# Kernel tuning notes

Measured on AMD Instinct MI355X. Metric: run time of the kernel, lower is better.

## Reference

```python
import jax, jax.numpy as jnp
import numpy as np

WIDTH = 1024

def setup_inputs() -> dict:
    key = jax.random.key(0)
    ks = jax.random.split(key, 5)
    x = jax.random.normal(ks[0], (4, 4096, WIDTH), dtype=jnp.float32)
    # LayerNorm params
    ln_gamma = jnp.ones((WIDTH,), dtype=jnp.float32)
    ln_beta = jnp.zeros((WIDTH,), dtype=jnp.float32)
    # Linear params (torch nn.Linear init: U(-1/sqrt(fan_in), 1/sqrt(fan_in)))
    bound = 1.0 / np.sqrt(WIDTH)
    w1 = jax.random.uniform(ks[1], (WIDTH, WIDTH), jnp.float32, -bound, bound)
    b1 = jax.random.uniform(ks[2], (WIDTH,), jnp.float32, -bound, bound)
    w2 = jax.random.uniform(ks[3], (WIDTH, WIDTH), jnp.float32, -bound, bound)
    b2 = jax.random.uniform(ks[4], (WIDTH,), jnp.float32, -bound, bound)
    return {"x": x, "ln_gamma": ln_gamma, "ln_beta": ln_beta,
            "w1": w1, "b1": b1, "w2": w2, "b2": b2}

def _layernorm(x, gamma, beta, eps=1e-5):
    mu = jnp.mean(x, axis=-1, keepdims=True)
    var = jnp.mean(jnp.square(x - mu), axis=-1, keepdims=True)
    return (x - mu) * jax.lax.rsqrt(var + eps) * gamma + beta

def reference(x, ln_gamma, ln_beta, w1, b1, w2, b2):
    # Pre-norm residual MLP: x + W2 @ gelu(W1 @ LN(x) + b1) + b2
    h = _layernorm(x, ln_gamma, ln_beta)
    h = jnp.einsum('bsd,ed->bse', h, w1) + b1  # w stored as [out, in] like torch
    h = jax.nn.gelu(h, approximate=False)      # torch nn.GELU default = exact erf
    # dropout p=0.0 -> identity
    h = jnp.einsum('bsd,ed->bse', h, w2) + b2
    return x + h
```

## Files before the change

kernel.cpp:

```cpp
#include <hip/hip_runtime.h>
#include <hip/hip_bf16.h>
#include <math.h>

typedef __bf16 bf16x8 __attribute__((ext_vector_type(8)));
typedef float f32x4 __attribute__((ext_vector_type(4)));

#define GAS __attribute__((address_space(1)))
#define LAS __attribute__((address_space(3)))

static __device__ __forceinline__ void load16(const void* g, void* l) {
    __builtin_amdgcn_global_load_lds((const GAS void*)g, (LAS void*)l, 16, 0, 0);
}

struct __align__(8) bh4 { __hip_bfloat16 x, y, z, w; };

__global__ __launch_bounds__(256) void ln_kernel(
        const float* __restrict__ x, const float* __restrict__ gamma,
        const float* __restrict__ beta, __hip_bfloat16* __restrict__ out) {
    const int row  = (blockIdx.x << 2) + (threadIdx.x >> 6);
    const int lane = threadIdx.x & 63;
    const float4* px = (const float4*)(x + (size_t)row * 1024);
    float4 v[4];
    float s = 0.f;
#pragma unroll
    for (int i = 0; i < 4; ++i) {
        v[i] = px[lane + (i << 6)];
        s += v[i].x + v[i].y + v[i].z + v[i].w;
    }
#pragma unroll
    for (int o = 32; o; o >>= 1) s += __shfl_xor(s, o, 64);
    const float mu = s * (1.0f / 1024.0f);
    float vs = 0.f;
#pragma unroll
    for (int i = 0; i < 4; ++i) {
        float a = v[i].x - mu, b = v[i].y - mu, c = v[i].z - mu, d = v[i].w - mu;
        vs += a * a + b * b + c * c + d * d;
    }
#pragma unroll
    for (int o = 32; o; o >>= 1) vs += __shfl_xor(vs, o, 64);
    const float rs = rsqrtf(vs * (1.0f / 1024.0f) + 1e-5f);
    const float4* pg = (const float4*)gamma;
    const float4* pb = (const float4*)beta;
    bh4* po = (bh4*)(out + (size_t)row * 1024);
#pragma unroll
    for (int i = 0; i < 4; ++i) {
        const int idx = lane + (i << 6);
        float4 g = pg[idx], bb = pb[idx];
        bh4 r;
        r.x = __float2bfloat16((v[i].x - mu) * rs * g.x + bb.x);
        r.y = __float2bfloat16((v[i].y - mu) * rs * g.y + bb.y);
        r.z = __float2bfloat16((v[i].z - mu) * rs * g.z + bb.z);
        r.w = __float2bfloat16((v[i].w - mu) * rs * g.w + bb.w);
        po[idx] = r;
    }
}

__global__ __launch_bounds__(256) void cvt_kernel(
        const float* __restrict__ w1, const float* __restrict__ w2,
        __hip_bfloat16* __restrict__ o1, __hip_bfloat16* __restrict__ o2) {
    const int i = blockIdx.x * 256 + threadIdx.x;
    float4 a = ((const float4*)w1)[i];
    float4 b = ((const float4*)w2)[i];
    bh4 r1, r2;
    r1.x = __float2bfloat16(a.x); r1.y = __float2bfloat16(a.y);
    r1.z = __float2bfloat16(a.z); r1.w = __float2bfloat16(a.w);
    r2.x = __float2bfloat16(b.x); r2.y = __float2bfloat16(b.y);
    r2.z = __float2bfloat16(b.z); r2.w = __float2bfloat16(b.w);
    ((bh4*)o1)[i] = r1;
    ((bh4*)o2)[i] = r2;
}

template <int EPI>
__global__ __launch_bounds__(256) void gemm_kernel(
        const __hip_bfloat16* __restrict__ A,
        const __hip_bfloat16* __restrict__ B,
        const float* __restrict__ bias,
        const float* __restrict__ resid,
        __hip_bfloat16* __restrict__ outb,
        float* __restrict__ outf) {
    constexpr int K = 1024, N = 1024;
    __shared__ __align__(16) __hip_bfloat16 sA[128 * 32];
    __shared__ __align__(16) __hip_bfloat16 sB[128 * 32];

    const int tid  = threadIdx.x;
    const int lane = tid & 63;
    const int w    = tid >> 6;
    const int wm   = (w >> 1) * 64;
    const int wn   = (w & 1) * 64;
    const int bm   = blockIdx.y * 128;
    const int bn   = blockIdx.x * 128;

    const int lr = tid >> 2;
    const int lc = (tid & 3) * 8;
    const __hip_bfloat16* ga = A + (size_t)(bm + lr) * K + lc;
    const __hip_bfloat16* gb = B + (size_t)(bn + lr) * K + lc;
    char* la = (char*)sA + tid * 16;
    char* lb = (char*)sB + tid * 16;

    f32x4 acc[4][4] = {};

    const int fr = lane & 15;
    const int fk = (lane >> 4) * 8;

    for (int kt = 0; kt < K; kt += 32) {
        load16(ga + kt,                 la);
        load16(ga + kt + (size_t)64*K,  la + 4096);
        load16(gb + kt,                 lb);
        load16(gb + kt + (size_t)64*K,  lb + 4096);
        __syncthreads();
        bf16x8 af[4], bfr[4];
#pragma unroll
        for (int i = 0; i < 4; ++i) {
            af[i]  = *(const bf16x8*)&sA[(wm + i * 16 + fr) * 32 + fk];
            bfr[i] = *(const bf16x8*)&sB[(wn + i * 16 + fr) * 32 + fk];
        }
#pragma unroll
        for (int i = 0; i < 4; ++i)
#pragma unroll
            for (int j = 0; j < 4; ++j)
                acc[i][j] = __builtin_amdgcn_mfma_f32_16x16x32_bf16(af[i], bfr[j], acc[i][j], 0, 0, 0);
        __syncthreads();
    }

    const int cr = (lane >> 4) * 4;
    const int cc = lane & 15;
#pragma unroll
    for (int i = 0; i < 4; ++i) {
#pragma unroll
        for (int r = 0; r < 4; ++r) {
            const size_t grow = (size_t)(bm + wm + i * 16 + cr + r);
#pragma unroll
            for (int j = 0; j < 4; ++j) {
                const int gcol = bn + wn + j * 16 + cc;
                float v = acc[i][j][r] + bias[gcol];
                if (EPI == 0) {
                    float g = 0.5f * v * (1.0f + erff(v * 0.70710678118654752f));
                    outb[grow * N + gcol] = __float2bfloat16(g);
                } else {
                    outf[grow * N + gcol] = v + resid[grow * N + gcol];
                }
            }
        }
    }
}

extern "C" void kernel_launch(void* const* d_in, const int* in_sizes, int n_in,
                              void* d_out, int out_size, void* d_ws, size_t ws_size,
                              hipStream_t stream) {
    const float* x     = (const float*)d_in[0];
    const float* gamma = (const float*)d_in[1];
    const float* beta  = (const float*)d_in[2];
    const float* w1    = (const float*)d_in[3];
    const float* b1    = (const float*)d_in[4];
    const float* w2    = (const float*)d_in[5];
    const float* b2    = (const float*)d_in[6];
    float* out = (float*)d_out;

    const int M = in_sizes[0] / 1024;

    char* ws = (char*)d_ws;
    __hip_bfloat16* hn  = (__hip_bfloat16*)ws;
    __hip_bfloat16* h1  = (__hip_bfloat16*)(ws + (size_t)M * 2048);
    __hip_bfloat16* w1b = (__hip_bfloat16*)(ws + (size_t)M * 4096);
    __hip_bfloat16* w2b = (__hip_bfloat16*)(ws + (size_t)M * 4096 + 2097152);

    ln_kernel<<<M / 4, 256, 0, stream>>>(x, gamma, beta, hn);
    cvt_kernel<<<1024, 256, 0, stream>>>(w1, w2, w1b, w2b);
    gemm_kernel<0><<<dim3(8, M / 128), 256, 0, stream>>>(hn, w1b, b1, nullptr, h1, nullptr);
    gemm_kernel<1><<<dim3(8, M / 128), 256, 0, stream>>>(h1, w2b, b2, x, nullptr, out);
}
```

Measured before the change: 255.1 us.

## Fuse prep kernels, deepen GEMM K-tile, swizzle LDS layout, vectorize epilogue

Merges the LayerNorm and weight-conversion kernels into one launch. The GEMM now uses a 64-wide K tile with an LDS layout that matches the MFMA fragments, so fragment loads become contiguous per-lane 16-byte reads. B rows are permuted so each lane owns four consecutive output columns, which allows vectorized bias, residual and output accesses. The grid axes are swapped so consecutive blocks walk along M, and launch bounds request 4 blocks per CU. Doubling LDS to 32KB per block may limit occupancy.

```diff
diff --git a/kernel.cpp b/kernel.cpp
--- a/kernel.cpp
+++ b/kernel.cpp
@@ -14,9 +14,24 @@
 
 struct __align__(8) bh4 { __hip_bfloat16 x, y, z, w; };
 
-__global__ __launch_bounds__(256) void ln_kernel(
+__global__ __launch_bounds__(256) void pre_kernel(
         const float* __restrict__ x, const float* __restrict__ gamma,
-        const float* __restrict__ beta, __hip_bfloat16* __restrict__ out) {
+        const float* __restrict__ beta, const float* __restrict__ w1,
+        const float* __restrict__ w2, __hip_bfloat16* __restrict__ hn,
+        __hip_bfloat16* __restrict__ w1b, __hip_bfloat16* __restrict__ w2b, int nln) {
+    if ((int)blockIdx.x >= nln) {
+        const int i = (blockIdx.x - nln) * 256 + threadIdx.x;
+        float4 a = ((const float4*)w1)[i];
+        float4 b = ((const float4*)w2)[i];
+        bh4 r1, r2;
+        r1.x = __float2bfloat16(a.x); r1.y = __float2bfloat16(a.y);
+        r1.z = __float2bfloat16(a.z); r1.w = __float2bfloat16(a.w);
+        r2.x = __float2bfloat16(b.x); r2.y = __float2bfloat16(b.y);
+        r2.z = __float2bfloat16(b.z); r2.w = __float2bfloat16(b.w);
+        ((bh4*)w1b)[i] = r1;
+        ((bh4*)w2b)[i] = r2;
+        return;
+    }
     const int row  = (blockIdx.x << 2) + (threadIdx.x >> 6);
     const int lane = threadIdx.x & 63;
     const float4* px = (const float4*)(x + (size_t)row * 1024);
@@ -41,7 +56,7 @@
     const float rs = rsqrtf(vs * (1.0f / 1024.0f) + 1e-5f);
     const float4* pg = (const float4*)gamma;
     const float4* pb = (const float4*)beta;
-    bh4* po = (bh4*)(out + (size_t)row * 1024);
+    bh4* po = (bh4*)(hn + (size_t)row * 1024);
 #pragma unroll
     for (int i = 0; i < 4; ++i) {
         const int idx = lane + (i << 6);
@@ -55,23 +70,8 @@
     }
 }
 
-__global__ __launch_bounds__(256) void cvt_kernel(
-        const float* __restrict__ w1, const float* __restrict__ w2,
-        __hip_bfloat16* __restrict__ o1, __hip_bfloat16* __restrict__ o2) {
-    const int i = blockIdx.x * 256 + threadIdx.x;
-    float4 a = ((const float4*)w1)[i];
-    float4 b = ((const float4*)w2)[i];
-    bh4 r1, r2;
-    r1.x = __float2bfloat16(a.x); r1.y = __float2bfloat16(a.y);
-    r1.z = __float2bfloat16(a.z); r1.w = __float2bfloat16(a.w);
-    r2.x = __float2bfloat16(b.x); r2.y = __float2bfloat16(b.y);
-    r2.z = __float2bfloat16(b.z); r2.w = __float2bfloat16(b.w);
-    ((bh4*)o1)[i] = r1;
-    ((bh4*)o2)[i] = r2;
-}
-
 template <int EPI>
-__global__ __launch_bounds__(256) void gemm_kernel(
+__global__ __launch_bounds__(256, 4) void gemm_kernel(
         const __hip_bfloat16* __restrict__ A,
         const __hip_bfloat16* __restrict__ B,
         const float* __restrict__ bias,
@@ -79,66 +79,82 @@
         __hip_bfloat16* __restrict__ outb,
         float* __restrict__ outf) {
     constexpr int K = 1024, N = 1024;
-    __shared__ __align__(16) __hip_bfloat16 sA[128 * 32];
-    __shared__ __align__(16) __hip_bfloat16 sB[128 * 32];
+    __shared__ __align__(16) char sA[16384];
+    __shared__ __align__(16) char sB[16384];
 
     const int tid  = threadIdx.x;
     const int lane = tid & 63;
     const int w    = tid >> 6;
     const int wm   = (w >> 1) * 64;
     const int wn   = (w & 1) * 64;
-    const int bm   = blockIdx.y * 128;
-    const int bn   = blockIdx.x * 128;
+    const int bm   = blockIdx.x * 128;
+    const int bn   = blockIdx.y * 128;
 
-    const int lr = tid >> 2;
-    const int lc = (tid & 3) * 8;
-    const __hip_bfloat16* ga = A + (size_t)(bm + lr) * K + lc;
-    const __hip_bfloat16* gb = B + (size_t)(bn + lr) * K + lc;
-    char* la = (char*)sA + tid * 16;
-    char* lb = (char*)sB + tid * 16;
+    const int f = lane & 15;
+    const int h = lane >> 4;
+
+    const __hip_bfloat16* gA[4];
+    const __hip_bfloat16* gB[4];
+#pragma unroll
+    for (int q = 0; q < 4; ++q) {
+        const int u  = q * 4 + w;
+        const int rg = u >> 1, c = u & 1;
+        gA[q] = A + (size_t)(bm + rg * 16 + f) * K + c * 32 + h * 8;
+        const int cg = u >> 3, j = (u >> 1) & 3;
+        gB[q] = B + (size_t)(bn + cg * 64 + f * 4 + j) * K + c * 32 + h * 8;
+    }
+    char* lA = sA + tid * 16;
+    char* lB = sB + tid * 16;
 
     f32x4 acc[4][4] = {};
 
-    const int fr = lane & 15;
-    const int fk = (lane >> 4) * 8;
-
-    for (int kt = 0; kt < K; kt += 32) {
-        load16(ga + kt,                 la);
-        load16(ga + kt + (size_t)64*K,  la + 4096);
-        load16(gb + kt,                 lb);
-        load16(gb + kt + (size_t)64*K,  lb + 4096);
+    for (int kt = 0; kt < K; kt += 64) {
+#pragma unroll
+        for (int q = 0; q < 4; ++q) {
+            load16(gA[q] + kt, lA + q * 4096);
+            load16(gB[q] + kt, lB + q * 4096);
+        }
         __syncthreads();
-        bf16x8 af[4], bfr[4];
 #pragma unroll
-        for (int i = 0; i < 4; ++i) {
-            af[i]  = *(const bf16x8*)&sA[(wm + i * 16 + fr) * 32 + fk];
-            bfr[i] = *(const bf16x8*)&sB[(wn + i * 16 + fr) * 32 + fk];
-        }
+        for (int c = 0; c < 2; ++c) {
+            bf16x8 af[4], bf[4];
 #pragma unroll
-        for (int i = 0; i < 4; ++i)
+            for (int i = 0; i < 4; ++i)
+                af[i] = *(const bf16x8*)(sA + ((((wm >> 4) + i) * 2 + c) << 10) + lane * 16);
 #pragma unroll
             for (int j = 0; j < 4; ++j)
-                acc[i][j] = __builtin_amdgcn_mfma_f32_16x16x32_bf16(af[i], bfr[j], acc[i][j], 0, 0, 0);
+                bf[j] = *(const bf16x8*)(sB + ((((wn >> 4) + j) * 2 + c) << 10) + lane * 16);
+#pragma unroll
+            for (int i = 0; i < 4; ++i)
+#pragma unroll
+                for (int j = 0; j < 4; ++j)
+                    acc[i][j] = __builtin_amdgcn_mfma_f32_16x16x32_bf16(af[i], bf[j], acc[i][j], 0, 0, 0);
+        }
         __syncthreads();
     }
 
-    const int cr = (lane >> 4) * 4;
-    const int cc = lane & 15;
+    const float4 bias4 = *(const float4*)(bias + bn + wn + f * 4);
+    const int colb = bn + wn + f * 4;
 #pragma unroll
     for (int i = 0; i < 4; ++i) {
 #pragma unroll
         for (int r = 0; r < 4; ++r) {
-            const size_t grow = (size_t)(bm + wm + i * 16 + cr + r);
-#pragma unroll
-            for (int j = 0; j < 4; ++j) {
-                const int gcol = bn + wn + j * 16 + cc;
-                float v = acc[i][j][r] + bias[gcol];
-                if (EPI == 0) {
-                    float g = 0.5f * v * (1.0f + erff(v * 0.70710678118654752f));
-                    outb[grow * N + gcol] = __float2bfloat16(g);
-                } else {
-                    outf[grow * N + gcol] = v + resid[grow * N + gcol];
-                }
+            const size_t grow = (size_t)(bm + wm + i * 16 + h * 4 + r);
+            float v0 = acc[i][0][r] + bias4.x;
+            float v1 = acc[i][1][r] + bias4.y;
+            float v2 = acc[i][2][r] + bias4.z;
+            float v3 = acc[i][3][r] + bias4.w;
+            if (EPI == 0) {
+                bh4 o;
+                o.x = __float2bfloat16(0.5f * v0 * (1.0f + erff(v0 * 0.70710678118654752f)));
+                o.y = __float2bfloat16(0.5f * v1 * (1.0f + erff(v1 * 0.70710678118654752f)));
+                o.z = __float2bfloat16(0.5f * v2 * (1.0f + erff(v2 * 0.70710678118654752f)));
+                o.w = __float2bfloat16(0.5f * v3 * (1.0f + erff(v3 * 0.70710678118654752f)));
+                *(bh4*)(outb + grow * N + colb) = o;
+            } else {
+                const float4 rs = *(const float4*)(resid + grow * N + colb);
+                float4 o = {v0 + rs.x, v1 + rs.y, v2 + rs.z, v3 + rs.w};
+                *(float4*)(outf + grow * N + colb) = o;
             }
         }
     }
@@ -164,8 +180,8 @@
     __hip_bfloat16* w1b = (__hip_bfloat16*)(ws + (size_t)M * 4096);
     __hip_bfloat16* w2b = (__hip_bfloat16*)(ws + (size_t)M * 4096 + 2097152);
 
-    ln_kernel<<<M / 4, 256, 0, stream>>>(x, gamma, beta, hn);
-    cvt_kernel<<<1024, 256, 0, stream>>>(w1, w2, w1b, w2b);
-    gemm_kernel<0><<<dim3(8, M / 128), 256, 0, stream>>>(hn, w1b, b1, nullptr, h1, nullptr);
-    gemm_kernel<1><<<dim3(8, M / 128), 256, 0, stream>>>(h1, w2b, b2, x, nullptr, out);
+    const int nln = M / 4;
+    pre_kernel<<<nln + 1024, 256, 0, stream>>>(x, gamma, beta, w1, w2, hn, w1b, w2b, nln);
+    gemm_kernel<0><<<dim3(M / 128, 8), 256, 0, stream>>>(hn, w1b, b1, nullptr, h1, nullptr);
+    gemm_kernel<1><<<dim3(M / 128, 8), 256, 0, stream>>>(h1, w2b, b2, x, nullptr, out);
 }
```

Measured after the change: 319.1 us. 1.25x slower.
